# Kernel optimization log

Measured on AMD Instinct MI355X. Metric: run time of the kernel, lower is better.

The kernel has to match this reference:

```python
import jax, jax.numpy as jnp
import numpy as np

B, T1, T2 = 8, 512, 128
LA = 128            # len_alphabet
E = LA // 2         # embedding_size = GRU units = conv channels
DL = 256            # lstm_outs feature dim


def gru_seq(x, mask, K, R, b):
    """Keras GRU (reset_after=True) with masking. x:(B,T,E) mask:(B,T) -> (B,T,U)."""
    u = R.shape[0]
    xg = jnp.einsum('bte,eu->btu', x, K) + b[0]  # precompute input gates (B,T,3U)

    def step(carry, inp):
        h, y_prev = carry
        xt, mt = inp
        rg = h @ R + b[1]
        xz, xr, xh = jnp.split(xt, 3, axis=-1)
        rz, rr, rh = jnp.split(rg, 3, axis=-1)
        z = jax.nn.sigmoid(xz + rz)
        r = jax.nn.sigmoid(xr + rr)
        hh = jnp.tanh(xh + r * rh)
        h_new = z * h + (1.0 - z) * hh
        m = mt[:, None]
        h_out = jnp.where(m, h_new, h)
        y = jnp.where(m, h_new, y_prev)  # masked steps copy previous output
        return (h_out, y), y

    h0 = jnp.zeros((x.shape[0], u), x.dtype)
    _, ys = jax.lax.scan(step, (h0, h0), (jnp.swapaxes(xg, 0, 1), mask.T))
    return jnp.swapaxes(ys, 0, 1)


def setup_inputs() -> dict:
    key = jax.random.key(0)
    ks = jax.random.split(key, 15)
    s = 0.05
    inp = {
        'lstm_outs': jax.random.normal(ks[0], (B, T1, DL), jnp.float32),
        'char_seq': jax.random.randint(ks[1], (B, T2), 1, LA + 1, jnp.int32),  # no pad -> mask all True
        'emb_table': jax.random.normal(ks[2], (LA + 1, E), jnp.float32) * s,
        'Kf': jax.random.normal(ks[3], (E, 3 * E), jnp.float32) * s,
        'Rf': jax.random.normal(ks[4], (E, 3 * E), jnp.float32) * s,
        'bf': jnp.zeros((2, 3 * E), jnp.float32),
        'Kb': jax.random.normal(ks[5], (E, 3 * E), jnp.float32) * s,
        'Rb': jax.random.normal(ks[6], (E, 3 * E), jnp.float32) * s,
        'bb': jnp.zeros((2, 3 * E), jnp.float32),
        'w_char': jax.random.normal(ks[7], (DL + 2 * E + 2, 1), jnp.float32) * s,
        'b_char': jnp.zeros((1,), jnp.float32),
        'conv1_w': jax.random.normal(ks[8], (2, 2 * E, E), jnp.float32) * s,
        'conv1_b': jnp.zeros((E,), jnp.float32),
        'conv2_w': jax.random.normal(ks[9], (2, E, E), jnp.float32) * s,
        'conv2_b': jnp.zeros((E,), jnp.float32),
    }
    return inp


def reference(lstm_outs, char_seq, emb_table, Kf, Rf, bf, Kb, Rb, bb,
              w_char, b_char, conv1_w, conv1_b, conv2_w, conv2_b):
    emb = emb_table[char_seq]                 # (B,T2,E)
    mask = char_seq != 0
    fwd = gru_seq(emb, mask, Kf, Rf, bf)
    bwd = gru_seq(emb[:, ::-1], mask[:, ::-1], Kb, Rb, bb)[:, ::-1]
    ctx = jnp.concatenate([fwd, bwd], axis=-1)  # (B,T2,2E) contexted_chars

    t1, t2 = lstm_outs.shape[1], ctx.shape[1]
    dl, dc = lstm_outs.shape[2], ctx.shape[2]
    # Dense(1) over concat([lstms, contexts, time_idx, char_idx]) decomposed per part
    w_l = w_char[:dl, 0]
    w_c = w_char[dl:dl + dc, 0]
    w_t = w_char[dl + dc, 0]
    w_i = w_char[dl + dc + 1, 0]
    score = (jnp.einsum('btd,d->bt', lstm_outs, w_l)[:, :, None]
             + jnp.einsum('bsd,d->bs', ctx, w_c)[:, None, :]
             + w_t * jnp.arange(t1, dtype=lstm_outs.dtype)[None, :, None]
             + w_i * jnp.arange(t2, dtype=lstm_outs.dtype)[None, None, :]
             + b_char[0])
    char_weights = score[..., None]           # (B,T1,T2,1)

    weighted = char_weights * ctx[:, None, :, :]  # (B,T1,T2,2E)
    # Conv1D kernel=2, valid, over char axis (-2)
    c1 = (jnp.einsum('btsc,co->btso', weighted[:, :, :-1], conv1_w[0])
          + jnp.einsum('btsc,co->btso', weighted[:, :, 1:], conv1_w[1]) + conv1_b)
    c2 = (jnp.einsum('btsc,co->btso', c1[:, :, :-1], conv2_w[0])
          + jnp.einsum('btsc,co->btso', c1[:, :, 1:], conv2_w[1]) + conv2_b)
    final_embedding = jnp.max(c2, axis=-2)    # (B,T1,E)
    return final_embedding, char_weights
```

## Files before the change

### kernel.cpp

```cpp
#include <hip/hip_runtime.h>
#include <hip/hip_bf16.h>
#include <math.h>

#define Bn 8
#define T1n 512
#define T2n 128
#define En 64
#define Gn 192
#define DLn 256

#define NEG_LOG2E  (-1.4426950408889634f)
#define TWO_LOG2E  (2.8853900817779268f)

typedef __attribute__((ext_vector_type(8))) short short8;
typedef __attribute__((ext_vector_type(4))) float float4v;

__device__ __forceinline__ float fast_rcp(float x) { return __builtin_amdgcn_rcpf(x); }

__device__ __forceinline__ float fast_exp2(float x) {
    float r;
    asm("v_exp_f32 %0, %1" : "=v"(r) : "v"(x));
    return r;
}

__device__ __forceinline__ unsigned short f32_to_bf16(float v) {
    unsigned u = __builtin_bit_cast(unsigned, v);
    u += 0x7FFFu + ((u >> 16) & 1u);
    return (unsigned short)(u >> 16);
}
__device__ __forceinline__ float bf16_to_f32(unsigned short s) {
    unsigned u = ((unsigned)s) << 16;
    return __builtin_bit_cast(float, u);
}

__device__ __forceinline__ void load_lds16(const void* g, void* l) {
    __builtin_amdgcn_global_load_lds(
        (const __attribute__((address_space(1))) unsigned int*)g,
        (__attribute__((address_space(3))) unsigned int*)l, 16, 0, 0);
}

__global__ __launch_bounds__(384) void k_pre(const int* __restrict__ char_seq,
                                             const float* __restrict__ emb_table,
                                             const float* __restrict__ Kf,
                                             const float* __restrict__ bf,
                                             const float* __restrict__ Kb,
                                             const float* __restrict__ bb,
                                             unsigned short* __restrict__ xgbf) {
    int bt = blockIdx.x;
    int b = bt >> 7, t = bt & 127;
    int tid = threadIdx.x;
    __shared__ __align__(16) float emb[En];
    if (tid < En) {
        int cs = char_seq[b * T2n + t];
        emb[tid] = emb_table[cs * En + tid];
    }
    __syncthreads();
    int d = tid / Gn;
    int j = tid - d * Gn;
    const float* K = d ? Kb : Kf;
    const float* bias = d ? bb : bf;
    float acc = bias[j];
    #pragma unroll
    for (int e = 0; e < En; ++e) acc = fmaf(emb[e], K[e * Gn + j], acc);
    if (j < 128) acc *= NEG_LOG2E;
    xgbf[((size_t)(d * Bn + b) * T2n + t) * Gn + j] = f32_to_bf16(acc);
}

__global__ __launch_bounds__(256) void k_scan(const unsigned short* __restrict__ xgbf,
                                              const float* __restrict__ Rf,
                                              const float* __restrict__ bf,
                                              const float* __restrict__ Rb,
                                              const float* __restrict__ bb,
                                              const int* __restrict__ char_seq,
                                              float* __restrict__ ctx) {
    int blk = blockIdx.x;
    int b = blk & 7, d = blk >> 3;
    int tid = threadIdx.x;
    int w = tid >> 6;
    int lane = tid & 63;
    int quad = lane >> 4, col = lane & 15;
    int u = w * 16 + col;

    __shared__ __align__(16) unsigned short xg_l[T2n * Gn];
    __shared__ __align__(16) unsigned short h0[En];
    __shared__ __align__(16) unsigned short h1[En];

    {
        const unsigned char* gb = (const unsigned char*)(xgbf + (size_t)(d * Bn + b) * T2n * Gn);
        unsigned char* lb = (unsigned char*)xg_l;
        #pragma unroll
        for (int i = 0; i < 12; ++i) {
            int o = (w * 12 + i) * 1024 + lane * 16;
            load_lds16(gb + o, lb + o);
        }
    }

    unsigned long long mlo = __ballot(char_seq[b * T2n + lane] != 0);
    unsigned long long mhi = __ballot(char_seq[b * T2n + 64 + lane] != 0);

    const float* R = d ? Rb : Rf;
    const float* bias = d ? bb : bf;
    short8 frag[3][2];
    float4v biasC[3];
    #pragma unroll
    for (int g = 0; g < 3; ++g) {
        int nt = g * 4 + w;
        #pragma unroll
        for (int kt = 0; kt < 2; ++kt) {
            short8 f;
            #pragma unroll
            for (int j = 0; j < 8; ++j) {
                float v = R[(kt * 32 + quad * 8 + j) * Gn + nt * 16 + col];
                if (g < 2) v *= NEG_LOG2E;
                f[j] = (short)f32_to_bf16(v);
            }
            frag[g][kt] = f;
        }
        float bv = bias[Gn + nt * 16 + col];
        if (g < 2) bv *= NEG_LOG2E;
        float4v c = {bv, 0.f, 0.f, 0.f};
        biasC[g] = c;
    }

    if (tid < En) h0[tid] = 0;
    float hreg = 0.f, y = 0.f;
    float* ctxb = ctx + (size_t)b * T2n * 128 + d * En;
    int i0 = d ? (T2n - 1) : 0;
    int istep = d ? -1 : 1;

    asm volatile("s_waitcnt vmcnt(0) lgkmcnt(0)" ::: "memory");
    __builtin_amdgcn_s_barrier();
    __builtin_amdgcn_sched_barrier(0);

    #define SCAN_STEP(CUR, NXT, STEP)                                              \
    {                                                                              \
        int idx = i0 + istep * (STEP);                                             \
        const short8* ap = (const short8*)(CUR);                                   \
        short8 a0 = ap[quad];                                                      \
        short8 a1 = ap[4 + quad];                                                  \
        int xb = idx * Gn + u;                                                     \
        unsigned short xzs = xg_l[xb];                                             \
        unsigned short xrs = xg_l[xb + 64];                                        \
        unsigned short xhs = xg_l[xb + 128];                                       \
        float4v aZ = __builtin_amdgcn_mfma_f32_16x16x32_bf16(a0, frag[0][0], biasC[0], 0, 0, 0); \
        float4v aR = __builtin_amdgcn_mfma_f32_16x16x32_bf16(a0, frag[1][0], biasC[1], 0, 0, 0); \
        float4v aH = __builtin_amdgcn_mfma_f32_16x16x32_bf16(a0, frag[2][0], biasC[2], 0, 0, 0); \
        aZ = __builtin_amdgcn_mfma_f32_16x16x32_bf16(a1, frag[0][1], aZ, 0, 0, 0); \
        aR = __builtin_amdgcn_mfma_f32_16x16x32_bf16(a1, frag[1][1], aR, 0, 0, 0); \
        aH = __builtin_amdgcn_mfma_f32_16x16x32_bf16(a1, frag[2][1], aH, 0, 0, 0); \
        float xz = bf16_to_f32(xzs), xr = bf16_to_f32(xrs), xh = bf16_to_f32(xhs); \
        float z = fast_rcp(1.f + fast_exp2(xz + aZ.x));                            \
        float r = fast_rcp(1.f + fast_exp2(xr + aR.x));                            \
        float a = fmaf(r, aH.x, xh);                                               \
        float hh = fmaf(-2.f, fast_rcp(1.f + fast_exp2(a * TWO_LOG2E)), 1.f);      \
        float hn = fmaf(z, hreg - hh, hh);                                         \
        bool m = (idx < 64) ? ((mlo >> idx) & 1ull) : ((mhi >> (idx - 64)) & 1ull);\
        if (m) { hreg = hn; y = hn; }                                              \
        if (quad == 0) {                                                           \
            (NXT)[u] = f32_to_bf16(hreg);                                          \
            ctxb[idx * 128 + u] = y;                                               \
        }                                                                          \
        asm volatile("s_waitcnt lgkmcnt(0)" ::: "memory");                         \
        __builtin_amdgcn_sched_barrier(0);                                         \
        __builtin_amdgcn_s_barrier();                                              \
        __builtin_amdgcn_sched_barrier(0);                                         \
    }

    for (int sp = 0; sp < T2n / 2; ++sp) {
        SCAN_STEP(h0, h1, 2 * sp);
        SCAN_STEP(h1, h0, 2 * sp + 1);
    }
    #undef SCAN_STEP
}

__global__ __launch_bounds__(128) void k_ctxw(const float* __restrict__ ctx,
                                              const float* __restrict__ conv1_w,
                                              const float* __restrict__ conv2_w,
                                              const float* __restrict__ w_char,
                                              const float* __restrict__ lstm,
                                              float* __restrict__ Am,
                                              float* __restrict__ Bm,
                                              float* __restrict__ Cm,
                                              float* __restrict__ sC,
                                              float* __restrict__ sL) {
    int bs = blockIdx.x;
    int tid = threadIdx.x;
    {
        int wv = tid >> 6, lane = tid & 63;
        const float4* wl = (const float4*)w_char;
        #pragma unroll
        for (int q = 0; q < 2; ++q) {
            int bt = bs * 4 + wv * 2 + q;
            const float4* row = (const float4*)(lstm + (size_t)bt * DLn);
            float4 r4 = row[lane];
            float4 w4 = wl[lane];
            float s = r4.x * w4.x + r4.y * w4.y + r4.z * w4.z + r4.w * w4.w;
            #pragma unroll
            for (int off = 32; off; off >>= 1) s += __shfl_down(s, off);
            if (lane == 0) sL[bt] = s;
        }
    }
    __shared__ float crow[128];
    __shared__ float p0[En], p1[En];
    crow[tid] = ctx[(size_t)bs * 128 + tid];
    __syncthreads();
    if (tid < 64) {
        float s = crow[tid] * w_char[DLn + tid] + crow[64 + tid] * w_char[DLn + 64 + tid];
        #pragma unroll
        for (int off = 32; off; off >>= 1) s += __shfl_down(s, off);
        if (tid == 0) sC[bs] = s;
    }
    int tap = tid >> 6, o = tid & 63;
    const float* W = conv1_w + tap * 128 * En;
    float acc = 0.f;
    #pragma unroll
    for (int c = 0; c < 128; ++c) acc = fmaf(crow[c], W[c * En + o], acc);
    if (tap == 0) p0[o] = acc; else p1[o] = acc;
    __syncthreads();
    const float* W20 = conv2_w;
    const float* W21 = conv2_w + En * En;
    if (tid < 64) {
        float a = 0.f, cm = 0.f;
        #pragma unroll
        for (int c = 0; c < En; ++c) {
            a  = fmaf(p0[c], W20[c * En + tid], a);
            cm = fmaf(p1[c], W21[c * En + tid], cm);
        }
        Am[(size_t)bs * En + tid] = a;
        Cm[(size_t)bs * En + tid] = cm;
    } else {
        int o2 = tid - 64;
        float bacc = 0.f;
        #pragma unroll
        for (int c = 0; c < En; ++c) {
            bacc = fmaf(p1[c], W20[c * En + o2], bacc);
            bacc = fmaf(p0[c], W21[c * En + o2], bacc);
        }
        Bm[(size_t)bs * En + o2] = bacc;
    }
}

__global__ __launch_bounds__(256) void k_final(const float* __restrict__ sL,
                                               const float* __restrict__ sC,
                                               const float* __restrict__ w_char,
                                               const float* __restrict__ b_char,
                                               const float* __restrict__ conv1_b,
                                               const float* __restrict__ conv2_w,
                                               const float* __restrict__ conv2_b,
                                               const float* __restrict__ Am,
                                               const float* __restrict__ Bm,
                                               const float* __restrict__ Cm,
                                               float* __restrict__ fe,
                                               float* __restrict__ cw) {
    int blk = blockIdx.x;
    int b = blk >> 6, ttile = blk & 63;
    int t0 = ttile * 8;
    int tid = threadIdx.x;
    float w_t = w_char[DLn + 128], w_i = w_char[DLn + 129], bc = b_char[0];
    __shared__ float sc8[8][T2n];
    if (tid < T2n) {
        int s = tid;
        float sCs = sC[b * T2n + s] + w_i * (float)s + bc;
        #pragma unroll
        for (int tt = 0; tt < 8; ++tt) {
            int t = t0 + tt;
            float v = sL[b * T1n + t] + sCs + w_t * (float)t;
            sc8[tt][s] = v;
            cw[((size_t)(b * T1n + t)) * T2n + s] = v;
        }
    }
    int o = tid & 63, p = tid >> 6;
    float bb2 = conv2_b[o];
    #pragma unroll
    for (int c = 0; c < En; ++c)
        bb2 += conv1_b[c] * (conv2_w[c * En + o] + conv2_w[En * En + c * En + o]);
    __syncthreads();

    float acc[8];
    #pragma unroll
    for (int tt = 0; tt < 8; ++tt) acc[tt] = -__builtin_inff();
    const float* Ab = Am + (size_t)(b * T2n) * En + o;
    const float* Bb = Bm + (size_t)(b * T2n) * En + o;
    const float* Cb = Cm + (size_t)(b * T2n) * En + o;
    for (int s = p; s < T2n - 2; s += 4) {
        float a  = Ab[s * En];
        float bm = Bb[(s + 1) * En];
        float cm = Cb[(s + 2) * En];
        #pragma unroll
        for (int tt = 0; tt < 8; ++tt) {
            float v = fmaf(sc8[tt][s], a,
                      fmaf(sc8[tt][s + 1], bm,
                      fmaf(sc8[tt][s + 2], cm, bb2)));
            acc[tt] = fmaxf(acc[tt], v);
        }
    }
    __shared__ float red[3][64][9];
    if (p) {
        #pragma unroll
        for (int tt = 0; tt < 8; ++tt) red[p - 1][o][tt] = acc[tt];
    }
    __syncthreads();
    if (p == 0) {
        #pragma unroll
        for (int tt = 0; tt < 8; ++tt) {
            float v = fmaxf(fmaxf(acc[tt], red[0][o][tt]),
                            fmaxf(red[1][o][tt], red[2][o][tt]));
            fe[((size_t)(b * T1n + t0 + tt)) * En + o] = v;
        }
    }
}

extern "C" void kernel_launch(void* const* d_in, const int* in_sizes, int n_in,
                              void* d_out, int out_size, void* d_ws, size_t ws_size,
                              hipStream_t stream) {
    const float* lstm      = (const float*)d_in[0];
    const int*   char_seq  = (const int*)d_in[1];
    const float* emb_table = (const float*)d_in[2];
    const float* Kf        = (const float*)d_in[3];
    const float* Rf        = (const float*)d_in[4];
    const float* bf        = (const float*)d_in[5];
    const float* Kb        = (const float*)d_in[6];
    const float* Rb        = (const float*)d_in[7];
    const float* bb        = (const float*)d_in[8];
    const float* w_char    = (const float*)d_in[9];
    const float* b_char    = (const float*)d_in[10];
    const float* conv1_w   = (const float*)d_in[11];
    const float* conv1_b   = (const float*)d_in[12];
    const float* conv2_w   = (const float*)d_in[13];
    const float* conv2_b   = (const float*)d_in[14];

    float* out = (float*)d_out;
    float* fe = out;
    float* cw = out + Bn * T1n * En;

    float* ws  = (float*)d_ws;
    unsigned short* xgbf = (unsigned short*)ws;
    float* ctx = ws + 98304;
    float* sC  = ctx + Bn * T2n * 128;
    float* sL  = sC + Bn * T2n;
    float* Am  = sL + Bn * T1n;
    float* Bm  = Am + Bn * T2n * En;
    float* Cm  = Bm + Bn * T2n * En;

    k_pre <<<Bn * T2n, 384, 0, stream>>>(char_seq, emb_table, Kf, bf, Kb, bb, xgbf);
    k_scan<<<16, 256, 0, stream>>>(xgbf, Rf, bf, Rb, bb, char_seq, ctx);
    k_ctxw<<<Bn * T2n, 128, 0, stream>>>(ctx, conv1_w, conv2_w, w_char, lstm,
                                         Am, Bm, Cm, sC, sL);
    k_final<<<(Bn * T1n) / 8, 256, 0, stream>>>(sL, sC, w_char, b_char, conv1_b,
                                                conv2_w, conv2_b, Am, Bm, Cm, fe, cw);
}
```

Before: 141.1 us.

## Prefetch next GRU input gates, move lstm dot to k_pre, widen k_final

The scan kernel now loads the next step's precomputed input-gate values from LDS while the current step's MFMAs run, taking that LDS read off the serial recurrence chain. The lstm·w_char dot product moves from k_ctxw into k_pre, so k_ctxw does less work after the scan. k_final goes from 256 to 512 threads, splitting the char loop eight ways with a 4x unroll and a wider reduction. This raises register and LDS use and adds a bounds clamp on the prefetch index.

```diff
diff --git a/kernel.cpp b/kernel.cpp
--- a/kernel.cpp
+++ b/kernel.cpp
@@ -45,7 +45,10 @@
                                              const float* __restrict__ bf,
                                              const float* __restrict__ Kb,
                                              const float* __restrict__ bb,
-                                             unsigned short* __restrict__ xgbf) {
+                                             const float* __restrict__ lstm,
+                                             const float* __restrict__ w_char,
+                                             unsigned short* __restrict__ xgbf,
+                                             float* __restrict__ sL) {
     int bt = blockIdx.x;
     int b = bt >> 7, t = bt & 127;
     int tid = threadIdx.x;
@@ -53,6 +56,20 @@
     if (tid < En) {
         int cs = char_seq[b * T2n + t];
         emb[tid] = emb_table[cs * En + tid];
+    }
+    {
+        int wv = tid >> 6, lane = tid & 63;
+        if (wv < 4) {
+            int bt4 = bt * 4 + wv;
+            const float4* row = (const float4*)(lstm + (size_t)bt4 * DLn);
+            const float4* wl = (const float4*)w_char;
+            float4 r4 = row[lane];
+            float4 w4 = wl[lane];
+            float s = r4.x * w4.x + r4.y * w4.y + r4.z * w4.z + r4.w * w4.w;
+            #pragma unroll
+            for (int off = 32; off; off >>= 1) s += __shfl_down(s, off);
+            if (lane == 0) sL[bt4] = s;
+        }
     }
     __syncthreads();
     int d = tid / Gn;
@@ -132,23 +149,30 @@
     __builtin_amdgcn_s_barrier();
     __builtin_amdgcn_sched_barrier(0);
 
-    #define SCAN_STEP(CUR, NXT, STEP)                                              \
+    unsigned short xz_a = xg_l[i0 * Gn + u];
+    unsigned short xr_a = xg_l[i0 * Gn + u + 64];
+    unsigned short xh_a = xg_l[i0 * Gn + u + 128];
+    unsigned short xz_b, xr_b, xh_b;
+
+    #define SCAN_STEP(CUR, NXT, STEP, XCz, XCr, XCh, XNz, XNr, XNh)                \
     {                                                                              \
         int idx = i0 + istep * (STEP);                                             \
         const short8* ap = (const short8*)(CUR);                                   \
         short8 a0 = ap[quad];                                                      \
         short8 a1 = ap[4 + quad];                                                  \
-        int xb = idx * Gn + u;                                                     \
-        unsigned short xzs = xg_l[xb];                                             \
-        unsigned short xrs = xg_l[xb + 64];                                        \
-        unsigned short xhs = xg_l[xb + 128];                                       \
+        int idxn = idx + istep;                                                    \
+        if ((unsigned)idxn >= T2n) idxn = idx;                                     \
+        int xbn = idxn * Gn + u;                                                   \
+        XNz = xg_l[xbn];                                                           \
+        XNr = xg_l[xbn + 64];                                                      \
+        XNh = xg_l[xbn + 128];                                                     \
         float4v aZ = __builtin_amdgcn_mfma_f32_16x16x32_bf16(a0, frag[0][0], biasC[0], 0, 0, 0); \
         float4v aR = __builtin_amdgcn_mfma_f32_16x16x32_bf16(a0, frag[1][0], biasC[1], 0, 0, 0); \
         float4v aH = __builtin_amdgcn_mfma_f32_16x16x32_bf16(a0, frag[2][0], biasC[2], 0, 0, 0); \
         aZ = __builtin_amdgcn_mfma_f32_16x16x32_bf16(a1, frag[0][1], aZ, 0, 0, 0); \
         aR = __builtin_amdgcn_mfma_f32_16x16x32_bf16(a1, frag[1][1], aR, 0, 0, 0); \
         aH = __builtin_amdgcn_mfma_f32_16x16x32_bf16(a1, frag[2][1], aH, 0, 0, 0); \
-        float xz = bf16_to_f32(xzs), xr = bf16_to_f32(xrs), xh = bf16_to_f32(xhs); \
+        float xz = bf16_to_f32(XCz), xr = bf16_to_f32(XCr), xh = bf16_to_f32(XCh); \
         float z = fast_rcp(1.f + fast_exp2(xz + aZ.x));                            \
         float r = fast_rcp(1.f + fast_exp2(xr + aR.x));                            \
         float a = fmaf(r, aH.x, xh);                                               \
@@ -167,8 +191,8 @@
     }
 
     for (int sp = 0; sp < T2n / 2; ++sp) {
-        SCAN_STEP(h0, h1, 2 * sp);
-        SCAN_STEP(h1, h0, 2 * sp + 1);
+        SCAN_STEP(h0, h1, 2 * sp,     xz_a, xr_a, xh_a, xz_b, xr_b, xh_b);
+        SCAN_STEP(h1, h0, 2 * sp + 1, xz_b, xr_b, xh_b, xz_a, xr_a, xh_a);
     }
     #undef SCAN_STEP
 }
@@ -177,29 +201,12 @@
                                               const float* __restrict__ conv1_w,
                                               const float* __restrict__ conv2_w,
                                               const float* __restrict__ w_char,
-                                              const float* __restrict__ lstm,
                                               float* __restrict__ Am,
                                               float* __restrict__ Bm,
                                               float* __restrict__ Cm,
-                                              float* __restrict__ sC,
-                                              float* __restrict__ sL) {
+                                              float* __restrict__ sC) {
     int bs = blockIdx.x;
     int tid = threadIdx.x;
-    {
-        int wv = tid >> 6, lane = tid & 63;
-        const float4* wl = (const float4*)w_char;
-        #pragma unroll
-        for (int q = 0; q < 2; ++q) {
-            int bt = bs * 4 + wv * 2 + q;
-            const float4* row = (const float4*)(lstm + (size_t)bt * DLn);
-            float4 r4 = row[lane];
-            float4 w4 = wl[lane];
-            float s = r4.x * w4.x + r4.y * w4.y + r4.z * w4.z + r4.w * w4.w;
-            #pragma unroll
-            for (int off = 32; off; off >>= 1) s += __shfl_down(s, off);
-            if (lane == 0) sL[bt] = s;
-        }
-    }
     __shared__ float crow[128];
     __shared__ float p0[En], p1[En];
     crow[tid] = ctx[(size_t)bs * 128 + tid];
@@ -240,7 +247,7 @@
     }
 }
 
-__global__ __launch_bounds__(256) void k_final(const float* __restrict__ sL,
+__global__ __launch_bounds__(512) void k_final(const float* __restrict__ sL,
                                                const float* __restrict__ sC,
                                                const float* __restrict__ w_char,
                                                const float* __restrict__ b_char,
@@ -282,7 +289,8 @@
     const float* Ab = Am + (size_t)(b * T2n) * En + o;
     const float* Bb = Bm + (size_t)(b * T2n) * En + o;
     const float* Cb = Cm + (size_t)(b * T2n) * En + o;
-    for (int s = p; s < T2n - 2; s += 4) {
+    #pragma unroll 4
+    for (int s = p; s < T2n - 2; s += 8) {
         float a  = Ab[s * En];
         float bm = Bb[(s + 1) * En];
         float cm = Cb[(s + 2) * En];
@@ -294,7 +302,7 @@
             acc[tt] = fmaxf(acc[tt], v);
         }
     }
-    __shared__ float red[3][64][9];
+    __shared__ float red[7][64][9];
     if (p) {
         #pragma unroll
         for (int tt = 0; tt < 8; ++tt) red[p - 1][o][tt] = acc[tt];
@@ -303,8 +311,9 @@
     if (p == 0) {
         #pragma unroll
         for (int tt = 0; tt < 8; ++tt) {
-            float v = fmaxf(fmaxf(acc[tt], red[0][o][tt]),
-                            fmaxf(red[1][o][tt], red[2][o][tt]));
+            float v = acc[tt];
+            #pragma unroll
+            for (int q = 0; q < 7; ++q) v = fmaxf(v, red[q][o][tt]);
             fe[((size_t)(b * T1n + t0 + tt)) * En + o] = v;
         }
     }
@@ -342,10 +351,11 @@
     float* Bm  = Am + Bn * T2n * En;
     float* Cm  = Bm + Bn * T2n * En;
 
-    k_pre <<<Bn * T2n, 384, 0, stream>>>(char_seq, emb_table, Kf, bf, Kb, bb, xgbf);
+    k_pre <<<Bn * T2n, 384, 0, stream>>>(char_seq, emb_table, Kf, bf, Kb, bb,
+                                         lstm, w_char, xgbf, sL);
     k_scan<<<16, 256, 0, stream>>>(xgbf, Rf, bf, Rb, bb, char_seq, ctx);
-    k_ctxw<<<Bn * T2n, 128, 0, stream>>>(ctx, conv1_w, conv2_w, w_char, lstm,
-                                         Am, Bm, Cm, sC, sL);
-    k_final<<<(Bn * T1n) / 8, 256, 0, stream>>>(sL, sC, w_char, b_char, conv1_b,
+    k_ctxw<<<Bn * T2n, 128, 0, stream>>>(ctx, conv1_w, conv2_w, w_char,
+                                         Am, Bm, Cm, sC);
+    k_final<<<(Bn * T1n) / 8, 512, 0, stream>>>(sL, sC, w_char, b_char, conv1_b,
                                                 conv2_w, conv2_b, Am, Bm, Cm, fe, cw);
 }
```

Result: faster. 137.6 us (median of 2 runs) (-2.5%).
